# Performance work log

Measured on AMD Instinct MI355X. Metric: run time of the kernel, lower is better.

Reference implementation:

```python
import jax, jax.numpy as jnp
import numpy as np

START_TAG = 0
END_TAG = 63
NEG_INF = -10000.0


def setup_inputs() -> dict:
    key = jax.random.key(0)
    k1, k2, k3 = jax.random.split(key, 3)
    S, D, L = 32768, 1024, 64  # seq_len, feature_dim, num_labels
    feats = jax.random.normal(k1, (S, D), jnp.float32)
    W = jax.random.normal(k2, (L, D), jnp.float32) * 0.02  # nn.Linear weight [out,in]
    b = jnp.zeros((L,), jnp.float32)
    transitions = jax.random.normal(k3, (L, L), jnp.float32)
    transitions = transitions.at[START_TAG, :].set(NEG_INF).at[:, END_TAG].set(NEG_INF)
    return {"feats": feats, "W": W, "b": b, "transitions": transitions}


def reference(feats, W, b, transitions):
    # emissions: [S, L]
    emissions = feats @ W.T + b

    # Viterbi forward pass.  scores[j] after step t = best path score ending in label j.
    init_scores = transitions[:, START_TAG] + emissions[0]

    def step(scores, emit):
        # swt[j, i] = scores[i] + T[j, i]  (transition i -> j)
        swt = scores[None, :] + transitions  # [L, L]
        new_scores = emit + jnp.max(swt, axis=-1)
        back_ptr = jnp.argmax(swt, axis=-1)
        return new_scores, back_ptr

    final_scores, back_ptrs = jax.lax.scan(step, init_scores, emissions[1:])
    final_scores = final_scores + transitions[END_TAG]

    viterbi_score = jnp.max(final_scores)
    last_tag = jnp.argmax(final_scores)

    # Backtrack: tag[t-1] = back_ptrs[t-1][tag[t]] (back_ptrs[k] is for time k+1).
    def back(tag, bp):
        return bp[tag], tag

    first_tag, rest_tags = jax.lax.scan(back, last_tag, back_ptrs, reverse=True)
    tag_seq = jnp.concatenate([first_tag[None], rest_tags])  # [S]
    return viterbi_score, tag_seq
```

## Files before the change

kernel.cpp:

```cpp
#include <hip/hip_runtime.h>

#define S_LEN 32768
#define D_DIM 1024
#define L_LAB 64
#define LC 32
#define NCH (S_LEN / LC)
#define H_WARM 12
#define NSUP 32
#define SUPC 32

#define EM_OFF   0
#define BP_OFF   (S_LEN * 64 * 4)
#define MAPS_OFF (BP_OFF + S_LEN * 64)
#define BND_OFF  (MAPS_OFF + NCH * 64)
#define WIN_OFF  (BND_OFF + 1024)
#define END_OFF  (WIN_OFF + NCH * 4)
#define FIN_OFF  (END_OFF + NCH * 4)
#define WBF_OFF  (FIN_OFF + 256)

typedef __attribute__((ext_vector_type(8))) short short8;
typedef __attribute__((ext_vector_type(4))) float floatx4;

__device__ inline unsigned short f32_bf16_rne(float f) {
    unsigned v = __float_as_uint(f);
    v += 0x7FFFu + ((v >> 16) & 1u);
    return (unsigned short)(v >> 16);
}
__device__ inline int imax(int a, int b) { return a > b ? a : b; }

__global__ __launch_bounds__(256) void wconv_kernel(
        const float* __restrict__ W, unsigned short* __restrict__ Wbf) {
    int i = blockIdx.x * 256 + threadIdx.x;
    Wbf[i] = f32_bf16_rne(W[i]);
}

__global__ __launch_bounds__(256) __attribute__((amdgpu_waves_per_eu(2, 2)))
void emis_kernel(
        const float* __restrict__ feats, const unsigned short* __restrict__ Wbf,
        const float* __restrict__ bvec, float* __restrict__ em) {
    __shared__ __align__(16) unsigned short As[64 * 72];
    __shared__ __align__(16) unsigned short Bs[64 * 72];

    const int tid = threadIdx.x;
    const int lan = tid & 15;
    const int q   = (tid >> 4) & 3;
    const int w   = tid >> 6;
    const int row0 = blockIdx.x * 64;

    floatx4 acc[4];
#pragma unroll
    for (int nt = 0; nt < 4; ++nt) acc[nt] = (floatx4){0.f, 0.f, 0.f, 0.f};

    for (int kb = 0; kb < D_DIM; kb += 64) {
        __syncthreads();
#pragma unroll
        for (int i = 0; i < 4; ++i) {
            int gi = tid + i * 256;
            int m = gi >> 4, g = gi & 15;
            float4 v = *(const float4*)&feats[(size_t)(row0 + m) * D_DIM + kb + g * 4];
            unsigned h0 = f32_bf16_rne(v.x) | ((unsigned)f32_bf16_rne(v.y) << 16);
            unsigned h1 = f32_bf16_rne(v.z) | ((unsigned)f32_bf16_rne(v.w) << 16);
            *(uint2*)&As[m * 72 + g * 4] = (uint2){h0, h1};
        }
#pragma unroll
        for (int i = 0; i < 2; ++i) {
            int gi = tid + i * 256;
            int m = gi >> 3, g = gi & 7;
            *(uint4*)&Bs[m * 72 + g * 8] =
                *(const uint4*)&Wbf[(size_t)m * D_DIM + kb + g * 8];
        }
        __syncthreads();

#pragma unroll
        for (int cc = 0; cc < 2; ++cc) {
            int koff = cc * 32 + q * 8;
            int m_loc = w * 16 + lan;
            short8 av = *(const short8*)&As[m_loc * 72 + koff];
#pragma unroll
            for (int nt = 0; nt < 4; ++nt) {
                int label = nt * 16 + lan;
                short8 bv = *(const short8*)&Bs[label * 72 + koff];
                acc[nt] = __builtin_amdgcn_mfma_f32_16x16x32_bf16(av, bv, acc[nt], 0, 0, 0);
            }
        }
    }

#pragma unroll
    for (int nt = 0; nt < 4; ++nt) {
        int label = nt * 16 + lan;
        float bias = bvec[label];
#pragma unroll
        for (int r = 0; r < 4; ++r) {
            int row = row0 + w * 16 + q * 4 + r;
            em[(size_t)row * 64 + label] = acc[nt][r] + bias;
        }
    }
}

__global__ __launch_bounds__(64) __attribute__((amdgpu_waves_per_eu(1, 1)))
void fwd_chunks(
        const float* __restrict__ em, const float* __restrict__ T,
        unsigned char* __restrict__ bp, unsigned char* __restrict__ maps,
        float* __restrict__ win, float* __restrict__ endsc,
        float* __restrict__ finrow) {
    const int j = threadIdx.x;
    const int c = blockIdx.x;
    const int a = c * LC;
    const int bend = a + LC;

    float Trow[64];
#pragma unroll
    for (int i = 0; i < 16; ++i)
        ((float4*)Trow)[i] = ((const float4*)(T + j * 64))[i];
#pragma unroll
    for (int i = 0; i < 64; ++i) Trow[i] += 32768.0f;

    int t0 = a - 1 - H_WARM;
    if (t0 < 0) t0 = 0;

    float sc;
    if (t0 == 0) {
        sc = Trow[0] + (em[j] - 32768.0f);
    } else {
        sc = em[(size_t)t0 * 64 + j];
    }

    auto step = [&](float e) {
        int sci = __float_as_int(sc);
        float v0 = 0.f, v1 = 0.f;
#pragma unroll
        for (int k = 0; k < 16; ++k) {
            float a0 = __int_as_float(__builtin_amdgcn_readlane(sci, k)) + Trow[k];
            float a1 = __int_as_float(__builtin_amdgcn_readlane(sci, k + 16)) + Trow[k + 16];
            float a2 = __int_as_float(__builtin_amdgcn_readlane(sci, k + 32)) + Trow[k + 32];
            float a3 = __int_as_float(__builtin_amdgcn_readlane(sci, k + 48)) + Trow[k + 48];
            v0 = fmaxf(fmaxf(v0, a0), a1);
            v1 = fmaxf(fmaxf(v1, a2), a3);
        }
        sc = e + fmaxf(v0, v1);
    };

    int bi = 0;
    auto stepx = [&](float e) {
        int sci = __float_as_int(sc);
        int m0 = 0, m1 = 0;
#pragma unroll
        for (int k = 0; k < 16; ++k) {
            float a0 = __int_as_float(__builtin_amdgcn_readlane(sci, k)) + Trow[k];
            float a1 = __int_as_float(__builtin_amdgcn_readlane(sci, k + 16)) + Trow[k + 16];
            float a2 = __int_as_float(__builtin_amdgcn_readlane(sci, k + 32)) + Trow[k + 32];
            float a3 = __int_as_float(__builtin_amdgcn_readlane(sci, k + 48)) + Trow[k + 48];
            int k0 = (__float_as_int(a0) & ~63) | (63 - k);
            int k1 = (__float_as_int(a1) & ~63) | (63 - (k + 16));
            int k2 = (__float_as_int(a2) & ~63) | (63 - (k + 32));
            int k3 = (__float_as_int(a3) & ~63) | (63 - (k + 48));
            m0 = imax(imax(m0, k0), k1);
            m1 = imax(imax(m1, k2), k3);
        }
        int mm = imax(m0, m1);
        bi = (mm & 63) ^ 63;
        sc = e + __int_as_float((mm & ~63) | 32);
    };

    int t = t0 + 1;
    if (t < a) {
        float p0 = em[(size_t)(t + 0) * 64 + j] - 32768.0f;
        float p1 = em[(size_t)(t + 1) * 64 + j] - 32768.0f;
        float p2 = em[(size_t)(t + 2) * 64 + j] - 32768.0f;
        float p3 = em[(size_t)(t + 3) * 64 + j] - 32768.0f;
        for (; t + 3 < a; t += 4) {
            float n0 = em[(size_t)(t + 4) * 64 + j] - 32768.0f;
            float n1 = em[(size_t)(t + 5) * 64 + j] - 32768.0f;
            float n2 = em[(size_t)(t + 6) * 64 + j] - 32768.0f;
            float n3 = em[(size_t)(t + 7) * 64 + j] - 32768.0f;
            step(p0); step(p1); step(p2); step(p3);
            p0 = n0; p1 = n1; p2 = n2; p3 = n3;
        }
        for (; t < a; ++t) { step(p0); p0 = p1; p1 = p2; p2 = p3; }
    }
    if (c > 0 && j == 0) win[c] = sc;

    int fmap = j;
    t = (a > 0) ? a : 1;
    {
        float p0 = em[(size_t)(t + 0) * 64 + j] - 32768.0f;
        float p1 = em[(size_t)(t + 1) * 64 + j] - 32768.0f;
        float p2 = em[(size_t)(t + 2) * 64 + j] - 32768.0f;
        float p3 = em[(size_t)(t + 3) * 64 + j] - 32768.0f;
        for (; t + 3 < bend; t += 4) {
            int t4 = t + 4 > S_LEN - 1 ? S_LEN - 1 : t + 4;
            int t5 = t + 5 > S_LEN - 1 ? S_LEN - 1 : t + 5;
            int t6 = t + 6 > S_LEN - 1 ? S_LEN - 1 : t + 6;
            int t7 = t + 7 > S_LEN - 1 ? S_LEN - 1 : t + 7;
            float n0 = em[(size_t)t4 * 64 + j] - 32768.0f;
            float n1 = em[(size_t)t5 * 64 + j] - 32768.0f;
            float n2 = em[(size_t)t6 * 64 + j] - 32768.0f;
            float n3 = em[(size_t)t7 * 64 + j] - 32768.0f;
            stepx(p0); bp[(size_t)(t + 0) * 64 + j] = (unsigned char)bi;
            fmap = __builtin_amdgcn_ds_bpermute(bi << 2, fmap);
            stepx(p1); bp[(size_t)(t + 1) * 64 + j] = (unsigned char)bi;
            fmap = __builtin_amdgcn_ds_bpermute(bi << 2, fmap);
            stepx(p2); bp[(size_t)(t + 2) * 64 + j] = (unsigned char)bi;
            fmap = __builtin_amdgcn_ds_bpermute(bi << 2, fmap);
            stepx(p3); bp[(size_t)(t + 3) * 64 + j] = (unsigned char)bi;
            fmap = __builtin_amdgcn_ds_bpermute(bi << 2, fmap);
            p0 = n0; p1 = n1; p2 = n2; p3 = n3;
        }
        for (; t < bend; ++t) {
            stepx(p0); bp[(size_t)t * 64 + j] = (unsigned char)bi;
            fmap = __builtin_amdgcn_ds_bpermute(bi << 2, fmap);
            p0 = p1; p1 = p2; p2 = p3;
        }
    }

    maps[c * 64 + j] = (unsigned char)fmap;
    if (j == 0) endsc[c] = sc;
    if (c == NCH - 1) finrow[j] = sc;
}

__global__ __launch_bounds__(1024) void finish_kernel(
        const float* __restrict__ T, const float* __restrict__ win,
        const float* __restrict__ endsc, const float* __restrict__ finrow,
        const unsigned char* __restrict__ maps, float* __restrict__ out,
        unsigned char* __restrict__ bnd) {
    __shared__ unsigned char sm[NSUP * 64];
    __shared__ unsigned char sbl[NSUP];
    __shared__ float psum[16];
    const int tid = threadIdx.x;
    const int lane = tid & 63;
    const int wid = tid >> 6;

    float p = 0.f;
    if (tid >= 1 && tid < NCH) p = endsc[tid - 1] - win[tid];
#pragma unroll
    for (int off = 32; off; off >>= 1) p += __shfl_xor(p, off, 64);
    if (lane == 0) psum[wid] = p;

#pragma unroll
    for (int r = 0; r < 2; ++r) {
        int s = wid * 2 + r;
        int x = lane;
#pragma unroll 4
        for (int q = SUPC - 1; q >= 0; --q) {
            int mq = maps[(s * SUPC + q) * 64 + lane];
            x = __builtin_amdgcn_ds_bpermute(x << 2, mq);
        }
        sm[s * 64 + lane] = (unsigned char)x;
    }
    __syncthreads();

    if (tid < 64) {
        float part = 0.f;
#pragma unroll
        for (int i = 0; i < 16; ++i) part += psum[i];

        float f = finrow[lane] + T[63 * 64 + lane];
        float best = 0.f; int bt_ = 0;
#pragma unroll
        for (int k = 0; k < 64; ++k) {
            float fv = __int_as_float(__builtin_amdgcn_readlane(__float_as_int(f), k));
            if (k == 0) best = fv;
            else if (fv > best) { best = fv; bt_ = k; }
        }
        if (lane == 0) out[0] = best + part;

        int rows[NSUP];
#pragma unroll
        for (int s = 0; s < NSUP; ++s) rows[s] = sm[s * 64 + lane];
        int x = bt_;
        int sbv = 0;
        if (lane == NSUP - 1) sbv = x;
#pragma unroll
        for (int s = NSUP - 1; s >= 1; --s) {
            x = __builtin_amdgcn_readlane(rows[s], x);
            if (lane == s - 1) sbv = x;
        }
        if (lane < NSUP) sbl[lane] = (unsigned char)sbv;
    }
    __syncthreads();

#pragma unroll
    for (int r = 0; r < 2; ++r) {
        int s = wid * 2 + r;
        int rows[SUPC];
#pragma unroll
        for (int q = 1; q < SUPC; ++q)
            rows[q] = maps[(s * SUPC + q) * 64 + lane];
        int x = __builtin_amdgcn_readfirstlane((int)sbl[s]);
        int bv = 0;
        if (lane == SUPC - 1) bv = x;
#pragma unroll
        for (int q = SUPC - 1; q >= 1; --q) {
            x = __builtin_amdgcn_readlane(rows[q], x);
            if (lane == q - 1) bv = x;
        }
        if (lane < SUPC) bnd[s * SUPC + lane] = (unsigned char)bv;
    }
}

__global__ __launch_bounds__(64) void bt_fill(
        const unsigned char* __restrict__ bp, const unsigned char* __restrict__ bnd,
        float* __restrict__ out) {
    const int c = blockIdx.x;
    const int lane = threadIdx.x;
    int rows[LC];
#pragma unroll
    for (int tt = 1; tt < LC; ++tt)
        rows[tt] = bp[((size_t)c * LC + tt) * 64 + lane];
    int x = __builtin_amdgcn_readfirstlane((int)bnd[c]);
    int tv = 0;
    if (lane == LC - 1) tv = x;
#pragma unroll
    for (int tt = LC - 1; tt >= 1; --tt) {
        x = __builtin_amdgcn_readlane(rows[tt], x);
        if (lane == tt - 1) tv = x;
    }
    if (lane < LC) out[1 + c * LC + lane] = (float)tv;
}

extern "C" void kernel_launch(void* const* d_in, const int* in_sizes, int n_in,
                              void* d_out, int out_size, void* d_ws, size_t ws_size,
                              hipStream_t stream) {
    const float* feats = (const float*)d_in[0];
    const float* W     = (const float*)d_in[1];
    const float* b     = (const float*)d_in[2];
    const float* T     = (const float*)d_in[3];
    float* out = (float*)d_out;

    char* ws = (char*)d_ws;
    float*          em     = (float*)(ws + EM_OFF);
    unsigned char*  bp     = (unsigned char*)(ws + BP_OFF);
    unsigned char*  maps   = (unsigned char*)(ws + MAPS_OFF);
    unsigned char*  bnd    = (unsigned char*)(ws + BND_OFF);
    float*          win    = (float*)(ws + WIN_OFF);
    float*          endsc  = (float*)(ws + END_OFF);
    float*          finrow = (float*)(ws + FIN_OFF);
    unsigned short* Wbf    = (unsigned short*)(ws + WBF_OFF);

    wconv_kernel<<<(L_LAB * D_DIM) / 256, 256, 0, stream>>>(W, Wbf);
    emis_kernel<<<S_LEN / 64, 256, 0, stream>>>(feats, Wbf, b, em);
    fwd_chunks<<<NCH, 64, 0, stream>>>(em, T, bp, maps, win, endsc, finrow);
    finish_kernel<<<1, 1024, 0, stream>>>(T, win, endsc, finrow, maps, out, bnd);
    bt_fill<<<NCH, 64, 0, stream>>>(bp, bnd, out);
}
```

Before: 247.3 us.

## Load GEMM operands straight from global into MFMA registers and repack argmax keys

The emissions GEMM stops staging feats and W tiles through shared memory. Each lane now loads its own feats row segment, converts it to bf16 in registers, and reads the bf16 W fragments directly from global memory, which removes the __syncthreads barriers and the LDS round trips. In exchange, W loads are repeated per wave and depend on cache hits, and the waves_per_eu hint is dropped. Separately, the backpointer argmax key now shifts the float bits left and uses an unsigned max, then rebuilds the score from the high bits with a fixed exponent. This assumes the scores stay in a narrow positive range (the emissions carry a -32768 offset) and keeps the same instruction count.

```diff
diff --git a/kernel.cpp b/kernel.cpp
--- a/kernel.cpp
+++ b/kernel.cpp
@@ -26,7 +26,7 @@
     v += 0x7FFFu + ((v >> 16) & 1u);
     return (unsigned short)(v >> 16);
 }
-__device__ inline int imax(int a, int b) { return a > b ? a : b; }
+__device__ inline unsigned umax(unsigned a, unsigned b) { return a > b ? a : b; }
 
 __global__ __launch_bounds__(256) void wconv_kernel(
         const float* __restrict__ W, unsigned short* __restrict__ Wbf) {
@@ -34,54 +34,35 @@
     Wbf[i] = f32_bf16_rne(W[i]);
 }
 
-__global__ __launch_bounds__(256) __attribute__((amdgpu_waves_per_eu(2, 2)))
-void emis_kernel(
+__global__ __launch_bounds__(256) void emis_kernel(
         const float* __restrict__ feats, const unsigned short* __restrict__ Wbf,
         const float* __restrict__ bvec, float* __restrict__ em) {
-    __shared__ __align__(16) unsigned short As[64 * 72];
-    __shared__ __align__(16) unsigned short Bs[64 * 72];
-
     const int tid = threadIdx.x;
     const int lan = tid & 15;
     const int q   = (tid >> 4) & 3;
     const int w   = tid >> 6;
     const int row0 = blockIdx.x * 64;
+    const int m_loc = w * 16 + lan;
+    const float* arow = feats + (size_t)(row0 + m_loc) * D_DIM;
 
     floatx4 acc[4];
 #pragma unroll
     for (int nt = 0; nt < 4; ++nt) acc[nt] = (floatx4){0.f, 0.f, 0.f, 0.f};
 
-    for (int kb = 0; kb < D_DIM; kb += 64) {
-        __syncthreads();
-#pragma unroll
-        for (int i = 0; i < 4; ++i) {
-            int gi = tid + i * 256;
-            int m = gi >> 4, g = gi & 15;
-            float4 v = *(const float4*)&feats[(size_t)(row0 + m) * D_DIM + kb + g * 4];
-            unsigned h0 = f32_bf16_rne(v.x) | ((unsigned)f32_bf16_rne(v.y) << 16);
-            unsigned h1 = f32_bf16_rne(v.z) | ((unsigned)f32_bf16_rne(v.w) << 16);
-            *(uint2*)&As[m * 72 + g * 4] = (uint2){h0, h1};
-        }
-#pragma unroll
-        for (int i = 0; i < 2; ++i) {
-            int gi = tid + i * 256;
-            int m = gi >> 3, g = gi & 7;
-            *(uint4*)&Bs[m * 72 + g * 8] =
-                *(const uint4*)&Wbf[(size_t)m * D_DIM + kb + g * 8];
-        }
-        __syncthreads();
-
-#pragma unroll
-        for (int cc = 0; cc < 2; ++cc) {
-            int koff = cc * 32 + q * 8;
-            int m_loc = w * 16 + lan;
-            short8 av = *(const short8*)&As[m_loc * 72 + koff];
-#pragma unroll
-            for (int nt = 0; nt < 4; ++nt) {
-                int label = nt * 16 + lan;
-                short8 bv = *(const short8*)&Bs[label * 72 + koff];
-                acc[nt] = __builtin_amdgcn_mfma_f32_16x16x32_bf16(av, bv, acc[nt], 0, 0, 0);
-            }
+    for (int kb = 0; kb < D_DIM; kb += 32) {
+        const int koff = kb + q * 8;
+        float4 va = *(const float4*)&arow[koff];
+        float4 vb = *(const float4*)&arow[koff + 4];
+        union { short8 s; unsigned u[4]; } ua;
+        ua.u[0] = f32_bf16_rne(va.x) | ((unsigned)f32_bf16_rne(va.y) << 16);
+        ua.u[1] = f32_bf16_rne(va.z) | ((unsigned)f32_bf16_rne(va.w) << 16);
+        ua.u[2] = f32_bf16_rne(vb.x) | ((unsigned)f32_bf16_rne(vb.y) << 16);
+        ua.u[3] = f32_bf16_rne(vb.z) | ((unsigned)f32_bf16_rne(vb.w) << 16);
+#pragma unroll
+        for (int nt = 0; nt < 4; ++nt) {
+            int label = nt * 16 + lan;
+            short8 bv = *(const short8*)&Wbf[(size_t)label * D_DIM + koff];
+            acc[nt] = __builtin_amdgcn_mfma_f32_16x16x32_bf16(ua.s, bv, acc[nt], 0, 0, 0);
         }
     }
 
@@ -143,23 +124,23 @@
     int bi = 0;
     auto stepx = [&](float e) {
         int sci = __float_as_int(sc);
-        int m0 = 0, m1 = 0;
+        unsigned m0 = 0u, m1 = 0u;
 #pragma unroll
         for (int k = 0; k < 16; ++k) {
             float a0 = __int_as_float(__builtin_amdgcn_readlane(sci, k)) + Trow[k];
             float a1 = __int_as_float(__builtin_amdgcn_readlane(sci, k + 16)) + Trow[k + 16];
             float a2 = __int_as_float(__builtin_amdgcn_readlane(sci, k + 32)) + Trow[k + 32];
             float a3 = __int_as_float(__builtin_amdgcn_readlane(sci, k + 48)) + Trow[k + 48];
-            int k0 = (__float_as_int(a0) & ~63) | (63 - k);
-            int k1 = (__float_as_int(a1) & ~63) | (63 - (k + 16));
-            int k2 = (__float_as_int(a2) & ~63) | (63 - (k + 32));
-            int k3 = (__float_as_int(a3) & ~63) | (63 - (k + 48));
-            m0 = imax(imax(m0, k0), k1);
-            m1 = imax(imax(m1, k2), k3);
-        }
-        int mm = imax(m0, m1);
-        bi = (mm & 63) ^ 63;
-        sc = e + __int_as_float((mm & ~63) | 32);
+            unsigned k0 = ((unsigned)__float_as_int(a0) << 6) | (unsigned)(63 - k);
+            unsigned k1 = ((unsigned)__float_as_int(a1) << 6) | (unsigned)(63 - (k + 16));
+            unsigned k2 = ((unsigned)__float_as_int(a2) << 6) | (unsigned)(63 - (k + 32));
+            unsigned k3 = ((unsigned)__float_as_int(a3) << 6) | (unsigned)(63 - (k + 48));
+            m0 = umax(umax(m0, k0), k1);
+            m1 = umax(umax(m1, k2), k3);
+        }
+        unsigned mm = umax(m0, m1);
+        bi = (int)(mm & 63u) ^ 63;
+        sc = e + __uint_as_float((mm >> 6) | 0x44000000u);
     };
 
     int t = t0 + 1;
```

Result: no change. 252.1 us (+1.9%).
